# Kernel tuning notes

Measured on AMD Instinct MI355X. Metric: run time of the kernel, lower is better.

## Reference

```python
import jax, jax.numpy as jnp
import numpy as np

B, H, W, C = 8, 32, 32, 512
NUM_HEADS = 8
HEAD_DIM = C // NUM_HEADS
SCALE = HEAD_DIM ** -0.5


def setup_inputs() -> dict:
    key = jax.random.key(0)
    ks = jax.random.split(key, 10)
    s = 0.02
    return {
        "x": jax.random.normal(ks[0], (B, H, W, C), dtype=jnp.float32),
        "qkv_w": jax.random.normal(ks[1], (3 * C, C), dtype=jnp.float32) * s,
        "proj_w": jax.random.normal(ks[2], (C, C), dtype=jnp.float32) * s,
        "proj_b": jnp.zeros((C,), dtype=jnp.float32),
        "fconv_w": jax.random.normal(ks[3], (C,), dtype=jnp.float32) * s,
        "fconv_b": jnp.zeros((C,), dtype=jnp.float32),
        "freq_w": jnp.ones((C,), dtype=jnp.float32),
        "ln_g": jnp.ones((C,), dtype=jnp.float32),
        "ln_b": jnp.zeros((C,), dtype=jnp.float32),
        "mix_w": jnp.array([0.5, 0.5], dtype=jnp.float32),
    }


def _spatial(x, qkv_w, proj_w, proj_b):
    b, h, w, c = x.shape
    n = h * w
    xf = x.reshape(b, n, c)
    qkv = xf @ qkv_w.T                                   # [b,n,3c]
    qkv = qkv.reshape(b, n, 3, NUM_HEADS, HEAD_DIM)
    q, k, v = qkv[:, :, 0], qkv[:, :, 1], qkv[:, :, 2]   # [b,n,h,d]
    attn = jnp.einsum("bqhd,bkhd->bhqk", q, k) * SCALE
    attn = jax.nn.softmax(attn, axis=-1)
    out = jnp.einsum("bhqk,bkhd->bqhd", attn, v).reshape(b, n, c)
    out = out @ proj_w.T + proj_b
    return out.reshape(b, h, w, c)


def _fourier(x, fconv_w, fconv_b, freq_w, ln_g, ln_b):
    b, h, w, c = x.shape
    xc = jnp.transpose(x, (0, 3, 1, 2))                  # [b,c,h,w]
    xfft = jnp.fft.rfft2(xc, norm="ortho")               # [b,c,h,w//2+1] complex
    enhanced = xfft * freq_w[None, :, None, None]
    # depthwise 1x1 conv applied to real and imag separately: y = x*w + bias
    wc = fconv_w[None, :, None, None]
    bc = fconv_b[None, :, None, None]
    fconv = xfft * wc + bc * (1.0 + 1.0j)
    combined = enhanced + 0.1 * fconv
    xif = jnp.fft.irfft2(combined, s=(h, w), norm="ortho")  # [b,c,h,w]
    xf = jnp.transpose(xif, (0, 2, 3, 1))                # [b,h,w,c]
    mu = jnp.mean(xf, axis=-1, keepdims=True)
    var = jnp.var(xf, axis=-1, keepdims=True)
    return (xf - mu) / jnp.sqrt(var + 1e-5) * ln_g + ln_b


def reference(x, qkv_w, proj_w, proj_b, fconv_w, fconv_b, freq_w, ln_g, ln_b, mix_w):
    spatial = _spatial(x, qkv_w, proj_w, proj_b)
    fourier = _fourier(x, fconv_w, fconv_b, freq_w, ln_g, ln_b)
    weights = jax.nn.softmax(mix_w)
    return weights[0] * spatial + weights[1] * fourier
```

## Files before the change

### kernel.cpp

```cpp
#include <hip/hip_runtime.h>

typedef unsigned short u16;
typedef __attribute__((ext_vector_type(8))) short bfrag;
typedef __attribute__((ext_vector_type(4))) float f32x4;
typedef __attribute__((ext_vector_type(4))) int i32x4;
typedef __attribute__((ext_vector_type(4))) unsigned short us4;
typedef __attribute__((ext_vector_type(8))) unsigned short us8;

__device__ __forceinline__ u16 f2bf(float f){
  unsigned int u = __float_as_uint(f);
  u += 0x7fffu + ((u >> 16) & 1u);
  return (u16)(u >> 16);
}

__global__ __launch_bounds__(256) void cast_all(const float* __restrict__ x,
    const float* __restrict__ wq, const float* __restrict__ wp,
    u16* __restrict__ xb, u16* __restrict__ wqb, u16* __restrict__ wpb)
{
  long e = ((long)blockIdx.x * 256 + threadIdx.x) * 4;
  const float* src; u16* dst; long off;
  if (e < 4194304L)               { src = x;  dst = xb;  off = e; }
  else if (e < 4980736L)          { src = wq; dst = wqb; off = e - 4194304L; }
  else                            { src = wp; dst = wpb; off = e - 4980736L; }
  f32x4 v = *(const f32x4*)(src + off);
  us4 o; o[0]=f2bf(v[0]); o[1]=f2bf(v[1]); o[2]=f2bf(v[2]); o[3]=f2bf(v[3]);
  *(us4*)(dst + off) = o;
}

__device__ __forceinline__ void gemm_core_128(const u16* __restrict__ A,
    const u16* __restrict__ W, int K, int m0, int n0,
    u16* As, u16* Ws, f32x4 acc[4][4])
{
  const int t = threadIdx.x;
  const int lane = t & 63, wave = t >> 6;
  const int wr = wave >> 1, wc = wave & 1;
  const int l15 = lane & 15, l4 = lane >> 4;
  const int rx = l15 & 7;
  for (int k0 = 0; k0 < K; k0 += 64){
    __syncthreads();
    #pragma unroll
    for (int i = 0; i < 4; i++){
      int idx = t + i*256;
      int row = idx >> 3;
      int cl = ((idx & 7) ^ (row & 7)) * 8;
      __builtin_amdgcn_global_load_lds(
        (const __attribute__((address_space(1))) void*)(A + (long)(m0+row)*K + k0 + cl),
        (__attribute__((address_space(3))) void*)(As + idx*8), 16, 0, 0);
      __builtin_amdgcn_global_load_lds(
        (const __attribute__((address_space(1))) void*)(W + (long)(n0+row)*K + k0 + cl),
        (__attribute__((address_space(3))) void*)(Ws + idx*8), 16, 0, 0);
    }
    __syncthreads();
    #pragma unroll
    for (int kd = 0; kd < 2; kd++){
      bfrag af[4], wf[4];
      const int pc = ((kd*4 + l4) ^ rx) * 8;
      #pragma unroll
      for (int m = 0; m < 4; m++) af[m] = *(bfrag*)&As[(wr*64 + m*16 + l15)*64 + pc];
      #pragma unroll
      for (int n = 0; n < 4; n++) wf[n] = *(bfrag*)&Ws[(wc*64 + n*16 + l15)*64 + pc];
      #pragma unroll
      for (int m = 0; m < 4; m++)
        #pragma unroll
        for (int n = 0; n < 4; n++)
          acc[m][n] = __builtin_amdgcn_mfma_f32_16x16x32_bf16(af[m], wf[n], acc[m][n], 0, 0, 0);
    }
  }
}

__global__ __launch_bounds__(256) void gemm_qkv(const u16* __restrict__ A,
    const u16* __restrict__ W, u16* __restrict__ Qb, u16* __restrict__ Kb, u16* __restrict__ Vt)
{
  __shared__ __align__(16) u16 As[128*64];
  __shared__ __align__(16) u16 Ws[128*64];
  f32x4 acc[4][4] = {};
  const int m0 = blockIdx.y * 128, n0 = blockIdx.x * 128;
  gemm_core_128(A, W, 512, m0, n0, As, Ws, acc);
  const int lane = threadIdx.x & 63, wave = threadIdx.x >> 6;
  const int wr = wave >> 1, wc = wave & 1, l15 = lane & 15, l4 = lane >> 4;
  #pragma unroll
  for (int m = 0; m < 4; m++)
    #pragma unroll
    for (int n = 0; n < 4; n++){
      int col = n0 + wc*64 + n*16 + l15;
      int s = col >> 9, r9 = col & 511;
      int hh = r9 >> 6, dd = r9 & 63;
      int row0 = m0 + wr*64 + m*16 + l4*4;
      int bb = row0 >> 10, nn = row0 & 1023;
      if (s == 2){
        us4 o;
        #pragma unroll
        for (int r = 0; r < 4; r++) o[r] = f2bf(acc[m][n][r]);
        *(us4*)&Vt[((long)(bb*8 + hh)*64 + dd)*1024 + nn] = o;
      } else {
        u16* base = (s == 0) ? Qb : Kb;
        #pragma unroll
        for (int r = 0; r < 4; r++)
          base[((long)(bb*8 + hh)*1024 + nn + r)*64 + dd] = f2bf(acc[m][n][r]);
      }
    }
}

__global__ __launch_bounds__(256) void gemm_proj(const u16* __restrict__ A,
    const u16* __restrict__ W, const float* __restrict__ bias, float* __restrict__ C)
{
  __shared__ __align__(16) u16 As[128*64];
  __shared__ __align__(16) u16 Ws[128*64];
  f32x4 acc[4][4] = {};
  const int m0 = blockIdx.y * 128, n0 = blockIdx.x * 128;
  gemm_core_128(A, W, 512, m0, n0, As, Ws, acc);
  const int lane = threadIdx.x & 63, wave = threadIdx.x >> 6;
  const int wr = wave >> 1, wc = wave & 1, l15 = lane & 15, l4 = lane >> 4;
  #pragma unroll
  for (int m = 0; m < 4; m++)
    #pragma unroll
    for (int n = 0; n < 4; n++){
      int col = n0 + wc*64 + n*16 + l15;
      float bv = bias[col];
      #pragma unroll
      for (int r = 0; r < 4; r++){
        int row = m0 + wr*64 + m*16 + l4*4 + r;
        C[(long)row*512 + col] = acc[m][n][r] + bv;
      }
    }
}

__global__ __launch_bounds__(256) void attn_kernel(const u16* __restrict__ Qb,
    const u16* __restrict__ Kb, const u16* __restrict__ Vt, u16* __restrict__ attn_out)
{
  const int qt = blockIdx.x;
  const int bh = blockIdx.y;
  const int b = bh >> 3, h = bh & 7;
  const int t = threadIdx.x;
  const int wave = t >> 6, lane = t & 63;
  const int l15 = lane & 15, l4 = lane >> 4;
  __shared__ __align__(16) u16 Ks[64][72];
  __shared__ __align__(16) u16 Vs[64][72];
  __shared__ __align__(16) u16 Ps[4][16][72];

  bfrag aq[2];
  const u16* Qbase = Qb + ((long)bh*1024 + qt*64 + wave*16) * 64;
  #pragma unroll
  for (int kd = 0; kd < 2; kd++)
    aq[kd] = *(const bfrag*)(Qbase + l15*64 + kd*32 + l4*8);

  f32x4 accO[4] = {};
  float lsum[4] = {0.f, 0.f, 0.f, 0.f};
  const float cexp = 0.125f * 1.4426950408889634f;

  const u16* Kbh = Kb + (long)bh*1024*64;
  const u16* Vbh = Vt + (long)bh*64*1024;

  const int sr = t >> 3;
  const int sc = (t & 7) * 8;
  const int qrow = 2*(l15 >> 2) + 8*(l15 & 1) + ((l15 >> 1) & 1);
  i32x4 kreg[2], vreg[2];
  #pragma unroll
  for (int i = 0; i < 2; i++){
    int r = sr + i*32;
    kreg[i] = *(const i32x4*)(Kbh + (long)r*64 + sc);
    vreg[i] = *(const i32x4*)(Vbh + (long)r*1024 + sc);
  }

  for (int kt = 0; kt < 16; kt++){
    asm volatile("s_barrier" ::: "memory");
    #pragma unroll
    for (int i = 0; i < 2; i++){
      int r = sr + i*32;
      *(i32x4*)&Ks[r][sc] = kreg[i];
      *(i32x4*)&Vs[r][sc] = vreg[i];
    }
    if (kt < 15){
      #pragma unroll
      for (int i = 0; i < 2; i++){
        int r = sr + i*32;
        kreg[i] = *(const i32x4*)(Kbh + (long)((kt+1)*64 + r)*64 + sc);
        vreg[i] = *(const i32x4*)(Vbh + (long)r*1024 + (kt+1)*64 + sc);
      }
    }
    asm volatile("s_waitcnt lgkmcnt(0)\ns_barrier" ::: "memory");
    #pragma unroll
    for (int kf = 0; kf < 4; kf++){
      f32x4 a = {};
      #pragma unroll
      for (int kd = 0; kd < 2; kd++){
        bfrag bk = *(bfrag*)&Ks[kf*16 + l15][kd*32 + l4*8];
        a = __builtin_amdgcn_mfma_f32_16x16x32_bf16(aq[kd], bk, a, 0, 0, 0);
      }
      #pragma unroll
      for (int r = 0; r < 4; r++){
        float p = exp2f(a[r] * cexp);
        lsum[r] += p;
        int prow = 2*l4 + 8*(r & 1) + ((r >> 1) & 1);
        Ps[wave][prow][kf*16 + l15] = f2bf(p);
      }
    }
    #pragma unroll
    for (int h2 = 0; h2 < 2; h2++){
      bfrag pa = *(bfrag*)&Ps[wave][qrow][h2*32 + l4*8];
      #pragma unroll
      for (int df = 0; df < 4; df++){
        bfrag bv = *(bfrag*)&Vs[df*16 + l15][h2*32 + l4*8];
        accO[df] = __builtin_amdgcn_mfma_f32_16x16x32_bf16(pa, bv, accO[df], 0, 0, 0);
      }
    }
  }
  #pragma unroll
  for (int r = 0; r < 4; r++){
    #pragma unroll
    for (int off = 1; off < 16; off <<= 1) lsum[r] += __shfl_xor(lsum[r], off, 64);
    float inv = 1.0f / lsum[r];
    int nq = qt*64 + wave*16 + l4*4 + r;
    u16* dst = attn_out + ((long)(b*1024 + nq))*512 + h*64;
    #pragma unroll
    for (int df = 0; df < 4; df++)
      dst[df*16 + l15] = f2bf(accO[df][r] * inv);
  }
}

__global__ __launch_bounds__(256) void fourier_mix(const float* __restrict__ x,
    const float* __restrict__ spatial,
    const float* __restrict__ fconv_w, const float* __restrict__ fconv_b,
    const float* __restrict__ freq_w, const float* __restrict__ ln_g,
    const float* __restrict__ ln_b, const float* __restrict__ mix_w,
    float* __restrict__ out)
{
  const int row = blockIdx.x * 4 + (threadIdx.x >> 6);
  const int lane = threadIdx.x & 63;
  const int c0 = lane * 8;
  const float* xr = x + (long)row*512 + c0;
  f32x4 xlo = *(const f32x4*)xr;
  f32x4 xhi = *(const f32x4*)(xr + 4);
  float xv[8] = {xlo[0],xlo[1],xlo[2],xlo[3],xhi[0],xhi[1],xhi[2],xhi[3]};
  const int hh = (row >> 5) & 31, ww = row & 31;
  float pw = 0.0f;
  if (hh == 0){
    pw = 1.0f + ((ww & 1) ? -1.0f : 1.0f);
    for (int k = 1; k < 16; k++){
      float ang = 6.283185307179586f * (float)(k*ww) / 32.0f;
      pw += 2.0f * (__cosf(ang) - __sinf(ang));
    }
  }
  float sum = 0.0f, ssq = 0.0f;
  float xf[8];
  #pragma unroll
  for (int j = 0; j < 8; j++){
    int c = c0 + j;
    float s = freq_w[c] + 0.1f * fconv_w[c];
    float v = xv[j]*s + 0.1f * fconv_b[c] * pw;
    xf[j] = v; sum += v; ssq += v*v;
  }
  #pragma unroll
  for (int off = 1; off < 64; off <<= 1){
    sum += __shfl_xor(sum, off, 64);
    ssq += __shfl_xor(ssq, off, 64);
  }
  const float mean = sum * (1.0f/512.0f);
  const float var  = ssq * (1.0f/512.0f) - mean*mean;
  const float rstd = rsqrtf(var + 1e-5f);
  const float e0 = expf(mix_w[0]), e1 = expf(mix_w[1]);
  const float w0 = e0/(e0+e1), w1 = e1/(e0+e1);
  const float* sp = spatial + (long)row*512 + c0;
  f32x4 olo, ohi;
  #pragma unroll
  for (int j = 0; j < 8; j++){
    int c = c0 + j;
    float ln = (xf[j] - mean)*rstd*ln_g[c] + ln_b[c];
    float o = w0*sp[j] + w1*ln;
    if (j < 4) olo[j] = o; else ohi[j-4] = o;
  }
  float* od = out + (long)row*512 + c0;
  *(f32x4*)od = olo;
  *(f32x4*)(od + 4) = ohi;
}

extern "C" void kernel_launch(void* const* d_in, const int* in_sizes, int n_in,
                              void* d_out, int out_size, void* d_ws, size_t ws_size,
                              hipStream_t stream)
{
  const float* x       = (const float*)d_in[0];
  const float* qkv_w   = (const float*)d_in[1];
  const float* proj_w  = (const float*)d_in[2];
  const float* proj_b  = (const float*)d_in[3];
  const float* fconv_w = (const float*)d_in[4];
  const float* fconv_b = (const float*)d_in[5];
  const float* freq_w  = (const float*)d_in[6];
  const float* ln_g    = (const float*)d_in[7];
  const float* ln_b    = (const float*)d_in[8];
  const float* mix_w   = (const float*)d_in[9];

  char* ws = (char*)d_ws;
  u16*   xb      = (u16*)(ws + 0);
  u16*   wqb     = (u16*)(ws + 8388608);
  u16*   wpb     = (u16*)(ws + 9961472);
  u16*   Qb      = (u16*)(ws + 10485760);
  u16*   Kb      = (u16*)(ws + 18874368);
  u16*   Vt      = (u16*)(ws + 27262976);
  u16*   attn    = (u16*)(ws + 35651584);
  float* spatial = (float*)(ws + 44040192);
  float* outp    = (float*)d_out;

  cast_all<<<dim3(5120), dim3(256), 0, stream>>>(x, qkv_w, proj_w, xb, wqb, wpb);
  gemm_qkv<<<dim3(12, 64), dim3(256), 0, stream>>>(xb, wqb, Qb, Kb, Vt);
  attn_kernel<<<dim3(16, 64), dim3(256), 0, stream>>>(Qb, Kb, Vt, attn);
  gemm_proj<<<dim3(4, 64), dim3(256), 0, stream>>>(attn, wpb, proj_b, spatial);
  fourier_mix<<<dim3(2048), dim3(256), 0, stream>>>(x, spatial, fconv_w, fconv_b,
                                                    freq_w, ln_g, ln_b, mix_w, outp);
}
```

Measured before the change: 172.5 us.

## Use bf16 intermediates for spatial output and x in fourier mix; prescale Q

The projection GEMM now writes its spatial output in bf16 instead of fp32. The final fourier/mix kernel reads the bf16 copy of x and the bf16 spatial buffer, which halves its input traffic. In attention, the softmax scale and log2e factor are folded into Q once at load, so the per-element multiply before exp2 goes away. Software bf16 rounding is replaced by the hardware v_cvt_pk_bf16_f32 instruction. The cost is extra precision loss: the LayerNorm path now sees x rounded to bf16, and Q is rounded after scaling.

```diff
diff --git a/kernel.cpp b/kernel.cpp
--- a/kernel.cpp
+++ b/kernel.cpp
@@ -11,6 +11,14 @@
   unsigned int u = __float_as_uint(f);
   u += 0x7fffu + ((u >> 16) & 1u);
   return (u16)(u >> 16);
+}
+__device__ __forceinline__ float bf2f(u16 u){
+  return __uint_as_float(((unsigned)u) << 16);
+}
+__device__ __forceinline__ u16 cvt_bf16(float f){
+  unsigned r;
+  asm("v_cvt_pk_bf16_f32 %0, %1, %2" : "=v"(r) : "v"(f), "v"(f));
+  return (u16)r;
 }
 
 __global__ __launch_bounds__(256) void cast_all(const float* __restrict__ x,
@@ -102,7 +110,7 @@
 }
 
 __global__ __launch_bounds__(256) void gemm_proj(const u16* __restrict__ A,
-    const u16* __restrict__ W, const float* __restrict__ bias, float* __restrict__ C)
+    const u16* __restrict__ W, const float* __restrict__ bias, u16* __restrict__ C)
 {
   __shared__ __align__(16) u16 As[128*64];
   __shared__ __align__(16) u16 Ws[128*64];
@@ -120,7 +128,7 @@
       #pragma unroll
       for (int r = 0; r < 4; r++){
         int row = m0 + wr*64 + m*16 + l4*4 + r;
-        C[(long)row*512 + col] = acc[m][n][r] + bv;
+        C[(long)row*512 + col] = cvt_bf16(acc[m][n][r] + bv);
       }
     }
 }
@@ -138,15 +146,20 @@
   __shared__ __align__(16) u16 Vs[64][72];
   __shared__ __align__(16) u16 Ps[4][16][72];
 
+  const float qs = 0.125f * 1.4426950408889634f;
   bfrag aq[2];
   const u16* Qbase = Qb + ((long)bh*1024 + qt*64 + wave*16) * 64;
   #pragma unroll
-  for (int kd = 0; kd < 2; kd++)
-    aq[kd] = *(const bfrag*)(Qbase + l15*64 + kd*32 + l4*8);
+  for (int kd = 0; kd < 2; kd++){
+    bfrag q = *(const bfrag*)(Qbase + l15*64 + kd*32 + l4*8);
+    #pragma unroll
+    for (int j = 0; j < 8; j++)
+      q[j] = (short)cvt_bf16(bf2f((u16)q[j]) * qs);
+    aq[kd] = q;
+  }
 
   f32x4 accO[4] = {};
   float lsum[4] = {0.f, 0.f, 0.f, 0.f};
-  const float cexp = 0.125f * 1.4426950408889634f;
 
   const u16* Kbh = Kb + (long)bh*1024*64;
   const u16* Vbh = Vt + (long)bh*64*1024;
@@ -189,10 +202,10 @@
       }
       #pragma unroll
       for (int r = 0; r < 4; r++){
-        float p = exp2f(a[r] * cexp);
+        float p = exp2f(a[r]);
         lsum[r] += p;
         int prow = 2*l4 + 8*(r & 1) + ((r >> 1) & 1);
-        Ps[wave][prow][kf*16 + l15] = f2bf(p);
+        Ps[wave][prow][kf*16 + l15] = cvt_bf16(p);
       }
     }
     #pragma unroll
@@ -214,12 +227,12 @@
     u16* dst = attn_out + ((long)(b*1024 + nq))*512 + h*64;
     #pragma unroll
     for (int df = 0; df < 4; df++)
-      dst[df*16 + l15] = f2bf(accO[df][r] * inv);
-  }
-}
-
-__global__ __launch_bounds__(256) void fourier_mix(const float* __restrict__ x,
-    const float* __restrict__ spatial,
+      dst[df*16 + l15] = cvt_bf16(accO[df][r] * inv);
+  }
+}
+
+__global__ __launch_bounds__(256) void fourier_mix(const u16* __restrict__ xb,
+    const u16* __restrict__ spatialb,
     const float* __restrict__ fconv_w, const float* __restrict__ fconv_b,
     const float* __restrict__ freq_w, const float* __restrict__ ln_g,
     const float* __restrict__ ln_b, const float* __restrict__ mix_w,
@@ -228,10 +241,7 @@
   const int row = blockIdx.x * 4 + (threadIdx.x >> 6);
   const int lane = threadIdx.x & 63;
   const int c0 = lane * 8;
-  const float* xr = x + (long)row*512 + c0;
-  f32x4 xlo = *(const f32x4*)xr;
-  f32x4 xhi = *(const f32x4*)(xr + 4);
-  float xv[8] = {xlo[0],xlo[1],xlo[2],xlo[3],xhi[0],xhi[1],xhi[2],xhi[3]};
+  us8 xv8 = *(const us8*)(xb + (long)row*512 + c0);
   const int hh = (row >> 5) & 31, ww = row & 31;
   float pw = 0.0f;
   if (hh == 0){
@@ -247,7 +257,7 @@
   for (int j = 0; j < 8; j++){
     int c = c0 + j;
     float s = freq_w[c] + 0.1f * fconv_w[c];
-    float v = xv[j]*s + 0.1f * fconv_b[c] * pw;
+    float v = bf2f(xv8[j])*s + 0.1f * fconv_b[c] * pw;
     xf[j] = v; sum += v; ssq += v*v;
   }
   #pragma unroll
@@ -260,13 +270,13 @@
   const float rstd = rsqrtf(var + 1e-5f);
   const float e0 = expf(mix_w[0]), e1 = expf(mix_w[1]);
   const float w0 = e0/(e0+e1), w1 = e1/(e0+e1);
-  const float* sp = spatial + (long)row*512 + c0;
+  us8 sp8 = *(const us8*)(spatialb + (long)row*512 + c0);
   f32x4 olo, ohi;
   #pragma unroll
   for (int j = 0; j < 8; j++){
     int c = c0 + j;
     float ln = (xf[j] - mean)*rstd*ln_g[c] + ln_b[c];
-    float o = w0*sp[j] + w1*ln;
+    float o = w0*bf2f(sp8[j]) + w1*ln;
     if (j < 4) olo[j] = o; else ohi[j-4] = o;
   }
   float* od = out + (long)row*512 + c0;
@@ -290,20 +300,20 @@
   const float* mix_w   = (const float*)d_in[9];
 
   char* ws = (char*)d_ws;
-  u16*   xb      = (u16*)(ws + 0);
-  u16*   wqb     = (u16*)(ws + 8388608);
-  u16*   wpb     = (u16*)(ws + 9961472);
-  u16*   Qb      = (u16*)(ws + 10485760);
-  u16*   Kb      = (u16*)(ws + 18874368);
-  u16*   Vt      = (u16*)(ws + 27262976);
-  u16*   attn    = (u16*)(ws + 35651584);
-  float* spatial = (float*)(ws + 44040192);
-  float* outp    = (float*)d_out;
+  u16*   xb       = (u16*)(ws + 0);
+  u16*   wqb      = (u16*)(ws + 8388608);
+  u16*   wpb      = (u16*)(ws + 9961472);
+  u16*   Qb       = (u16*)(ws + 10485760);
+  u16*   Kb       = (u16*)(ws + 18874368);
+  u16*   Vt       = (u16*)(ws + 27262976);
+  u16*   attn     = (u16*)(ws + 35651584);
+  u16*   spatialb = (u16*)(ws + 44040192);
+  float* outp     = (float*)d_out;
 
   cast_all<<<dim3(5120), dim3(256), 0, stream>>>(x, qkv_w, proj_w, xb, wqb, wpb);
   gemm_qkv<<<dim3(12, 64), dim3(256), 0, stream>>>(xb, wqb, Qb, Kb, Vt);
   attn_kernel<<<dim3(16, 64), dim3(256), 0, stream>>>(Qb, Kb, Vt, attn);
-  gemm_proj<<<dim3(4, 64), dim3(256), 0, stream>>>(attn, wpb, proj_b, spatial);
-  fourier_mix<<<dim3(2048), dim3(256), 0, stream>>>(x, spatial, fconv_w, fconv_b,
+  gemm_proj<<<dim3(4, 64), dim3(256), 0, stream>>>(attn, wpb, proj_b, spatialb);
+  fourier_mix<<<dim3(2048), dim3(256), 0, stream>>>(xb, spatialb, fconv_w, fconv_b,
                                                     freq_w, ln_g, ln_b, mix_w, outp);
 }
```

After: 172.7 us. About the same (+0.1%).
